# Kernel tuning notes

Measured on AMD Instinct MI355X. Metric: run time of the kernel, lower is better.

Reference implementation:

```python
import jax, jax.numpy as jnp
import numpy as np

B = 16          # number of documents
PREV = 768      # prev_output_size (input embedding dim)
D = 256         # input_size after projection
LENGTHS = np.array([1024 + 128 * i for i in range(B)], dtype=np.int64)  # ragged doc lengths
T = int(LENGTHS.sum())      # 31744 total sentence embeddings
MAXLEN = int(LENGTHS.max()) # 2944 padded sequence length


def setup_inputs() -> dict:
    key = jax.random.key(0)
    k1, k2 = jax.random.split(key, 2)
    sent_embs = jax.random.normal(k1, (T, PREV), dtype=jnp.float32)
    W = jax.random.normal(k2, (PREV, D), dtype=jnp.float32) / np.float32(np.sqrt(PREV))
    b = jnp.zeros((D,), dtype=jnp.float32)
    return {
        "sent_embs": sent_embs,
        "W": W,
        "b": b,
        "lengths": jnp.asarray(LENGTHS),
        "max_len": MAXLEN,
    }


def reference(sent_embs, W, b, lengths, max_len):
    # emb_to_hidden_mapping: Linear(prev_output_size -> input_size)
    x = sent_embs @ W + b                      # [T, D]
    T_ = x.shape[0]
    Bn = lengths.shape[0]
    # Ragged -> padded scatter (replaces the Python index-building loop):
    # exclusive cumsum gives the start offset of each doc inside the concat.
    offs = jnp.concatenate([jnp.zeros((1,), lengths.dtype), jnp.cumsum(lengths)[:-1]])
    batch_ids = jnp.repeat(jnp.arange(Bn), lengths, total_repeat_length=T_)  # [T]
    within = jnp.arange(T_) - offs[batch_ids]                                # position inside doc
    tgt = batch_ids * max_len + within                                       # flat padded row index
    padded = jnp.zeros((Bn * max_len, x.shape[1]), x.dtype).at[tgt].set(x)
    # encoder is an injected opaque module; identity here -> padded seqs
    return padded.reshape(Bn, max_len, x.shape[1])  # [B, max_len, D]
```

## Files before the change

kernel.cpp:

```cpp
#include <hip/hip_runtime.h>
#include <hip/hip_bf16.h>


#define T_TOTAL 31744
#define K_DIM   768
#define N_DIM   256
#define MAXLEN  2944
#define NKT     24
#define NGEMM   496
#define NZERO   240

typedef __attribute__((ext_vector_type(8))) short    bf16x8;
typedef __attribute__((ext_vector_type(4))) float    f32x4;
typedef __attribute__((ext_vector_type(4))) unsigned u32x4;

__device__ __forceinline__ unsigned short f2bf(float f) {
  unsigned u = __builtin_bit_cast(unsigned, f);
  u += 0x7fffu + ((u >> 16) & 1u);
  return (unsigned short)(u >> 16);
}

__device__ __forceinline__ unsigned cvtpk(float lo, float hi) {
  unsigned r;
  asm("v_cvt_pk_bf16_f32 %0, %1, %2" : "=v"(r) : "v"(lo), "v"(hi));
  return r;
}

__device__ __forceinline__ void gload16(const void* g, void* l) {
  __builtin_amdgcn_global_load_lds(
      (const __attribute__((address_space(1))) unsigned int*)g,
      (__attribute__((address_space(3))) unsigned int*)l,
      16, 0, 0);
}

__global__ __launch_bounds__(256) void wt_tile(const float* __restrict__ W,
                                               unsigned short* __restrict__ Wt) {
  __shared__ float Wl[32][257];
  const int kt  = blockIdx.x;
  const int tid = threadIdx.x;

#pragma unroll
  for (int i = 0; i < 8; ++i) {
    const int idx = i * 256 + tid;
    const int row = idx >> 6;
    const int c4  = idx & 63;
    f32x4 v = *(const f32x4*)(W + (size_t)(kt * 32 + row) * N_DIM + c4 * 4);
    Wl[row][c4 * 4 + 0] = v[0];
    Wl[row][c4 * 4 + 1] = v[1];
    Wl[row][c4 * 4 + 2] = v[2];
    Wl[row][c4 * 4 + 3] = v[3];
  }
  __syncthreads();

#pragma unroll
  for (int h = 0; h < 4; ++h) {
    bf16x8 ov;
#pragma unroll
    for (int e = 0; e < 8; ++e) ov[e] = (short)f2bf(Wl[h * 8 + e][tid]);
    *(bf16x8*)(Wt + (((size_t)kt * 4 + h) * 256 + tid) * 8) = ov;
  }
}

__global__ __launch_bounds__(512, 4) void gemm_scatter(const float* __restrict__ A,
                                                       const unsigned short* __restrict__ Wt,
                                                       const float* __restrict__ bias,
                                                       float* __restrict__ out) {
  const int tid = threadIdx.x;

  if (blockIdx.x >= NGEMM) {
    const int z  = blockIdx.x - NGEMM;
    const int p0 = z * 64;
    int d = 0, c = 0;
    while (d < 15) {
      const int pad = 1920 - 128 * d;
      if (p0 < c + pad) break;
      c += pad; ++d;
    }
    const int len = 1024 + 128 * d;
    const size_t row0 = (size_t)d * MAXLEN + len + (p0 - c);
    float* dst = out + row0 * N_DIM;
    const f32x4 z4 = {0.f, 0.f, 0.f, 0.f};
#pragma unroll
    for (int j = 0; j < 8; ++j)
      *(f32x4*)(dst + (size_t)(j * 512 + tid) * 4) = z4;
    return;
  }

  __shared__ f32x4 AbV[2][256];
  __shared__ f32x4 BbV[2][1024];

  const int wid  = tid >> 6;
  const int lane = tid & 63;
  const int l15  = lane & 15;
  const int l4   = lane >> 4;
  const int wr   = wid >> 2;
  const int wc   = wid & 3;
  const int t0   = blockIdx.x * 64;

  int off = 0, doc = 0;
  while (doc < 15) {
    const int len = 1024 + 128 * doc;
    if (t0 < off + len) break;
    off += len; ++doc;
  }
  const long tgt0 = (long)doc * MAXLEN + (t0 - off);

  const int rowS = (tid & 255) >> 2;
  const int gS   = tid & 3;
  const float* pA = A + (size_t)(t0 + rowS) * K_DIM + gS * 8;
  const int awbyte = (gS * 64 + (rowS ^ (gS << 1))) * 16;

  const unsigned short* pB = Wt + (size_t)tid * 8;

  char* ldsA  = (char*)&AbV[0][0];
  char* ldsB  = (char*)&BbV[0][0];
  char* ldsBw = ldsB + wid * 1024;

  const int arow  = wr * 32 + l15;
  const int aoff0 = l4 * 1024 + ((arow ^ (l4 << 1)) * 16);
  const int boff  = l4 * 4096 + (wc * 64 + l15) * 16;

  f32x4 acc[2][4];
#pragma unroll
  for (int m = 0; m < 2; ++m)
#pragma unroll
    for (int n = 0; n < 4; ++n) acc[m][n] = f32x4{0.f, 0.f, 0.f, 0.f};

#define STAGE_B(buf, kt_)                                                \
  {                                                                      \
    gload16(pB + (size_t)(kt_) * 8192, ldsBw + (buf) * 16384);           \
    gload16(pB + (size_t)(kt_) * 8192 + 4096,                            \
            ldsBw + (buf) * 16384 + 8192);                               \
  }

#define WRITE_A(buf, La0, La1)                                           \
  {                                                                      \
    u32x4 u;                                                             \
    u[0] = cvtpk(La0[0], La0[1]); u[1] = cvtpk(La0[2], La0[3]);          \
    u[2] = cvtpk(La1[0], La1[1]); u[3] = cvtpk(La1[2], La1[3]);          \
    *(u32x4*)(ldsA + (buf) * 4096 + awbyte) = u;                         \
  }

#define COMPUTE(buf)                                                     \
  {                                                                      \
    const char* ab = ldsA + (buf) * 4096;                                \
    const char* bb = ldsB + (buf) * 16384 + boff;                        \
    bf16x8 bf0 = *(const bf16x8*)(bb);                                   \
    bf16x8 bf1 = *(const bf16x8*)(bb + 256);                             \
    bf16x8 bf2 = *(const bf16x8*)(bb + 512);                             \
    bf16x8 bf3 = *(const bf16x8*)(bb + 768);                             \
    bf16x8 af0 = *(const bf16x8*)(ab + aoff0);                           \
    bf16x8 af1 = *(const bf16x8*)(ab + aoff0 + 256);                     \
    acc[0][0] = __builtin_amdgcn_mfma_f32_16x16x32_bf16(af0, bf0, acc[0][0], 0, 0, 0); \
    acc[0][1] = __builtin_amdgcn_mfma_f32_16x16x32_bf16(af0, bf1, acc[0][1], 0, 0, 0); \
    acc[0][2] = __builtin_amdgcn_mfma_f32_16x16x32_bf16(af0, bf2, acc[0][2], 0, 0, 0); \
    acc[0][3] = __builtin_amdgcn_mfma_f32_16x16x32_bf16(af0, bf3, acc[0][3], 0, 0, 0); \
    acc[1][0] = __builtin_amdgcn_mfma_f32_16x16x32_bf16(af1, bf0, acc[1][0], 0, 0, 0); \
    acc[1][1] = __builtin_amdgcn_mfma_f32_16x16x32_bf16(af1, bf1, acc[1][1], 0, 0, 0); \
    acc[1][2] = __builtin_amdgcn_mfma_f32_16x16x32_bf16(af1, bf2, acc[1][2], 0, 0, 0); \
    acc[1][3] = __builtin_amdgcn_mfma_f32_16x16x32_bf16(af1, bf3, acc[1][3], 0, 0, 0); \
  }

  if (tid < 256) {
    f32x4 La0 = *(const f32x4*)(pA);
    f32x4 La1 = *(const f32x4*)(pA + 4);
    WRITE_A(0, La0, La1)
  }
  STAGE_B(0, 0)
  __syncthreads();

#pragma unroll 1
  for (int t = 0; t < NKT - 1; ++t) {
    f32x4 La0, La1;
    if (tid < 256) {
      La0 = *(const f32x4*)(pA + (t + 1) * 32);
      La1 = *(const f32x4*)(pA + (t + 1) * 32 + 4);
    }
    STAGE_B((t + 1) & 1, t + 1)
    COMPUTE(t & 1)
    if (tid < 256) WRITE_A((t + 1) & 1, La0, La1)
    __syncthreads();
  }
  COMPUTE((NKT - 1) & 1)

  float bc[4];
#pragma unroll
  for (int n = 0; n < 4; ++n) bc[n] = bias[wc * 64 + n * 16 + l15];

#pragma unroll
  for (int m = 0; m < 2; ++m)
#pragma unroll
    for (int n = 0; n < 4; ++n) {
      const size_t base = (size_t)(tgt0 + wr * 32 + m * 16 + l4 * 4) * N_DIM
                        + wc * 64 + n * 16 + l15;
#pragma unroll
      for (int j = 0; j < 4; ++j)
        out[base + (size_t)j * N_DIM] = acc[m][n][j] + bc[n];
    }
#undef STAGE_B
#undef WRITE_A
#undef COMPUTE
}

extern "C" void kernel_launch(void* const* d_in, const int* in_sizes, int n_in,
                              void* d_out, int out_size, void* d_ws, size_t ws_size,
                              hipStream_t stream) {
  const float* A    = (const float*)d_in[0];
  const float* W    = (const float*)d_in[1];
  const float* bias = (const float*)d_in[2];
  float* out = (float*)d_out;
  unsigned short* Wt = (unsigned short*)d_ws;

  wt_tile<<<24, 256, 0, stream>>>(W, Wt);
  gemm_scatter<<<NGEMM + NZERO, 512, 0, stream>>>(A, Wt, bias, out);
}
```

Baseline: 33.58 us.

## Shrink GEMM tile to 32 rows and load W fragments directly from global

Halves the row tile per block to 32 tokens with 256 threads (4 waves), doubling the GEMM grid. The LDS staging of the bf16 W tile via global_load_lds is removed, and each wave now loads its B fragments straight from global memory (L2-resident) into registers every k-step. This cuts LDS use and barrier work and raises block count for occupancy. The trade-off is more redundant global/L2 traffic for W, since it is no longer shared across waves through LDS, and load latency is exposed in the loop.

```diff
diff --git a/kernel.cpp b/kernel.cpp
--- a/kernel.cpp
+++ b/kernel.cpp
@@ -7,7 +7,7 @@
 #define N_DIM   256
 #define MAXLEN  2944
 #define NKT     24
-#define NGEMM   496
+#define NGEMM   992
 #define NZERO   240
 
 typedef __attribute__((ext_vector_type(8))) short    bf16x8;
@@ -24,13 +24,6 @@
   unsigned r;
   asm("v_cvt_pk_bf16_f32 %0, %1, %2" : "=v"(r) : "v"(lo), "v"(hi));
   return r;
-}
-
-__device__ __forceinline__ void gload16(const void* g, void* l) {
-  __builtin_amdgcn_global_load_lds(
-      (const __attribute__((address_space(1))) unsigned int*)g,
-      (__attribute__((address_space(3))) unsigned int*)l,
-      16, 0, 0);
 }
 
 __global__ __launch_bounds__(256) void wt_tile(const float* __restrict__ W,
@@ -61,7 +54,7 @@
   }
 }
 
-__global__ __launch_bounds__(512, 4) void gemm_scatter(const float* __restrict__ A,
+__global__ __launch_bounds__(256, 4) void gemm_scatter(const float* __restrict__ A,
                                                        const unsigned short* __restrict__ Wt,
                                                        const float* __restrict__ bias,
                                                        float* __restrict__ out) {
@@ -81,21 +74,18 @@
     float* dst = out + row0 * N_DIM;
     const f32x4 z4 = {0.f, 0.f, 0.f, 0.f};
 #pragma unroll
-    for (int j = 0; j < 8; ++j)
-      *(f32x4*)(dst + (size_t)(j * 512 + tid) * 4) = z4;
+    for (int j = 0; j < 16; ++j)
+      *(f32x4*)(dst + (size_t)(j * 256 + tid) * 4) = z4;
     return;
   }
 
-  __shared__ f32x4 AbV[2][256];
-  __shared__ f32x4 BbV[2][1024];
+  __shared__ f32x4 AbV[2][128];
 
   const int wid  = tid >> 6;
   const int lane = tid & 63;
   const int l15  = lane & 15;
   const int l4   = lane >> 4;
-  const int wr   = wid >> 2;
-  const int wc   = wid & 3;
-  const int t0   = blockIdx.x * 64;
+  const int t0   = blockIdx.x * 32;
 
   int off = 0, doc = 0;
   while (doc < 15) {
@@ -105,20 +95,17 @@
   }
   const long tgt0 = (long)doc * MAXLEN + (t0 - off);
 
-  const int rowS = (tid & 255) >> 2;
+  const int rowS = (tid & 127) >> 2;
   const int gS   = tid & 3;
   const float* pA = A + (size_t)(t0 + rowS) * K_DIM + gS * 8;
-  const int awbyte = (gS * 64 + (rowS ^ (gS << 1))) * 16;
+  const int awbyte = (gS * 32 + (rowS ^ (gS << 1))) * 16;
 
-  const unsigned short* pB = Wt + (size_t)tid * 8;
+  const int colB = wid * 64 + l15;
+  const unsigned short* pB = Wt + ((size_t)l4 * 256 + colB) * 8;
 
-  char* ldsA  = (char*)&AbV[0][0];
-  char* ldsB  = (char*)&BbV[0][0];
-  char* ldsBw = ldsB + wid * 1024;
+  char* ldsA = (char*)&AbV[0][0];
 
-  const int arow  = wr * 32 + l15;
-  const int aoff0 = l4 * 1024 + ((arow ^ (l4 << 1)) * 16);
-  const int boff  = l4 * 4096 + (wc * 64 + l15) * 16;
+  const int aoff0 = l4 * 512 + ((l15 ^ (l4 << 1)) * 16);
 
   f32x4 acc[2][4];
 #pragma unroll
@@ -126,80 +113,69 @@
 #pragma unroll
     for (int n = 0; n < 4; ++n) acc[m][n] = f32x4{0.f, 0.f, 0.f, 0.f};
 
-#define STAGE_B(buf, kt_)                                                \
-  {                                                                      \
-    gload16(pB + (size_t)(kt_) * 8192, ldsBw + (buf) * 16384);           \
-    gload16(pB + (size_t)(kt_) * 8192 + 4096,                            \
-            ldsBw + (buf) * 16384 + 8192);                               \
-  }
-
 #define WRITE_A(buf, La0, La1)                                           \
   {                                                                      \
     u32x4 u;                                                             \
     u[0] = cvtpk(La0[0], La0[1]); u[1] = cvtpk(La0[2], La0[3]);          \
     u[2] = cvtpk(La1[0], La1[1]); u[3] = cvtpk(La1[2], La1[3]);          \
-    *(u32x4*)(ldsA + (buf) * 4096 + awbyte) = u;                         \
+    *(u32x4*)(ldsA + (buf) * 2048 + awbyte) = u;                         \
   }
 
-#define COMPUTE(buf)                                                     \
-  {                                                                      \
-    const char* ab = ldsA + (buf) * 4096;                                \
-    const char* bb = ldsB + (buf) * 16384 + boff;                        \
-    bf16x8 bf0 = *(const bf16x8*)(bb);                                   \
-    bf16x8 bf1 = *(const bf16x8*)(bb + 256);                             \
-    bf16x8 bf2 = *(const bf16x8*)(bb + 512);                             \
-    bf16x8 bf3 = *(const bf16x8*)(bb + 768);                             \
-    bf16x8 af0 = *(const bf16x8*)(ab + aoff0);                           \
-    bf16x8 af1 = *(const bf16x8*)(ab + aoff0 + 256);                     \
-    acc[0][0] = __builtin_amdgcn_mfma_f32_16x16x32_bf16(af0, bf0, acc[0][0], 0, 0, 0); \
-    acc[0][1] = __builtin_amdgcn_mfma_f32_16x16x32_bf16(af0, bf1, acc[0][1], 0, 0, 0); \
-    acc[0][2] = __builtin_amdgcn_mfma_f32_16x16x32_bf16(af0, bf2, acc[0][2], 0, 0, 0); \
-    acc[0][3] = __builtin_amdgcn_mfma_f32_16x16x32_bf16(af0, bf3, acc[0][3], 0, 0, 0); \
-    acc[1][0] = __builtin_amdgcn_mfma_f32_16x16x32_bf16(af1, bf0, acc[1][0], 0, 0, 0); \
-    acc[1][1] = __builtin_amdgcn_mfma_f32_16x16x32_bf16(af1, bf1, acc[1][1], 0, 0, 0); \
-    acc[1][2] = __builtin_amdgcn_mfma_f32_16x16x32_bf16(af1, bf2, acc[1][2], 0, 0, 0); \
-    acc[1][3] = __builtin_amdgcn_mfma_f32_16x16x32_bf16(af1, bf3, acc[1][3], 0, 0, 0); \
-  }
-
-  if (tid < 256) {
+  if (tid < 128) {
     f32x4 La0 = *(const f32x4*)(pA);
     f32x4 La1 = *(const f32x4*)(pA + 4);
     WRITE_A(0, La0, La1)
   }
-  STAGE_B(0, 0)
   __syncthreads();
 
 #pragma unroll 1
-  for (int t = 0; t < NKT - 1; ++t) {
+  for (int t = 0; t < NKT; ++t) {
+    const unsigned short* pBt = pB + (size_t)t * 8192;
+    bf16x8 b0 = *(const bf16x8*)(pBt);
+    bf16x8 b1 = *(const bf16x8*)(pBt + 128);
+    bf16x8 b2 = *(const bf16x8*)(pBt + 256);
+    bf16x8 b3 = *(const bf16x8*)(pBt + 384);
+
     f32x4 La0, La1;
-    if (tid < 256) {
+    if (t < NKT - 1 && tid < 128) {
       La0 = *(const f32x4*)(pA + (t + 1) * 32);
       La1 = *(const f32x4*)(pA + (t + 1) * 32 + 4);
     }
-    STAGE_B((t + 1) & 1, t + 1)
-    COMPUTE(t & 1)
-    if (tid < 256) WRITE_A((t + 1) & 1, La0, La1)
-    __syncthreads();
+
+    const char* ab = ldsA + (t & 1) * 2048;
+    bf16x8 af0 = *(const bf16x8*)(ab + aoff0);
+    bf16x8 af1 = *(const bf16x8*)(ab + aoff0 + 256);
+
+    acc[0][0] = __builtin_amdgcn_mfma_f32_16x16x32_bf16(af0, b0, acc[0][0], 0, 0, 0);
+    acc[0][1] = __builtin_amdgcn_mfma_f32_16x16x32_bf16(af0, b1, acc[0][1], 0, 0, 0);
+    acc[0][2] = __builtin_amdgcn_mfma_f32_16x16x32_bf16(af0, b2, acc[0][2], 0, 0, 0);
+    acc[0][3] = __builtin_amdgcn_mfma_f32_16x16x32_bf16(af0, b3, acc[0][3], 0, 0, 0);
+    acc[1][0] = __builtin_amdgcn_mfma_f32_16x16x32_bf16(af1, b0, acc[1][0], 0, 0, 0);
+    acc[1][1] = __builtin_amdgcn_mfma_f32_16x16x32_bf16(af1, b1, acc[1][1], 0, 0, 0);
+    acc[1][2] = __builtin_amdgcn_mfma_f32_16x16x32_bf16(af1, b2, acc[1][2], 0, 0, 0);
+    acc[1][3] = __builtin_amdgcn_mfma_f32_16x16x32_bf16(af1, b3, acc[1][3], 0, 0, 0);
+
+    if (t < NKT - 1) {
+      if (tid < 128) WRITE_A((t + 1) & 1, La0, La1)
+      __syncthreads();
+    }
   }
-  COMPUTE((NKT - 1) & 1)
 
   float bc[4];
 #pragma unroll
-  for (int n = 0; n < 4; ++n) bc[n] = bias[wc * 64 + n * 16 + l15];
+  for (int n = 0; n < 4; ++n) bc[n] = bias[wid * 64 + n * 16 + l15];
 
 #pragma unroll
   for (int m = 0; m < 2; ++m)
 #pragma unroll
     for (int n = 0; n < 4; ++n) {
-      const size_t base = (size_t)(tgt0 + wr * 32 + m * 16 + l4 * 4) * N_DIM
-                        + wc * 64 + n * 16 + l15;
+      const size_t base = (size_t)(tgt0 + m * 16 + l4 * 4) * N_DIM
+                        + wid * 64 + n * 16 + l15;
 #pragma unroll
       for (int j = 0; j < 4; ++j)
         out[base + (size_t)j * N_DIM] = acc[m][n][j] + bc[n];
     }
-#undef STAGE_B
 #undef WRITE_A
-#undef COMPUTE
 }
 
 extern "C" void kernel_launch(void* const* d_in, const int* in_sizes, int n_in,
@@ -212,5 +188,5 @@
   unsigned short* Wt = (unsigned short*)d_ws;
 
   wt_tile<<<24, 256, 0, stream>>>(W, Wt);
-  gemm_scatter<<<NGEMM + NZERO, 512, 0, stream>>>(A, Wt, bias, out);
+  gemm_scatter<<<NGEMM + NZERO, 256, 0, stream>>>(A, Wt, bias, out);
 }
```

Measured after the change: 36.50 us. 8.7% more time.

## Double GEMM row tile to 128 rows per block with 4x4 MFMA per wave

Applied to the files above, without the earlier changes.

Each GEMM block now covers 128 token rows instead of 64, so the GEMM grid is halved. All 512 threads load the fp32 activations, and each wave runs a 4x4 grid of MFMA tiles per k-step. The LDS A buffer and its swizzle are widened to match, and the occupancy hint drops from 4 to 2 blocks. The aim is to reuse each staged bf16 W tile across twice as many rows, cutting L2 traffic for W and barrier overhead per row. The costs are fewer blocks (248 GEMM blocks on a 256-CU part), higher register use and lower occupancy, which can hurt latency hiding in what is largely a memory-bound kernel.

```diff
diff --git a/kernel.cpp b/kernel.cpp
--- a/kernel.cpp
+++ b/kernel.cpp
@@ -7,7 +7,7 @@
 #define N_DIM   256
 #define MAXLEN  2944
 #define NKT     24
-#define NGEMM   496
+#define NGEMM   248
 #define NZERO   240
 
 typedef __attribute__((ext_vector_type(8))) short    bf16x8;
@@ -61,7 +61,7 @@
   }
 }
 
-__global__ __launch_bounds__(512, 4) void gemm_scatter(const float* __restrict__ A,
+__global__ __launch_bounds__(512, 2) void gemm_scatter(const float* __restrict__ A,
                                                        const unsigned short* __restrict__ Wt,
                                                        const float* __restrict__ bias,
                                                        float* __restrict__ out) {
@@ -86,7 +86,7 @@
     return;
   }
 
-  __shared__ f32x4 AbV[2][256];
+  __shared__ f32x4 AbV[2][512];
   __shared__ f32x4 BbV[2][1024];
 
   const int wid  = tid >> 6;
@@ -95,7 +95,7 @@
   const int l4   = lane >> 4;
   const int wr   = wid >> 2;
   const int wc   = wid & 3;
-  const int t0   = blockIdx.x * 64;
+  const int t0   = blockIdx.x * 128;
 
   int off = 0, doc = 0;
   while (doc < 15) {
@@ -105,10 +105,10 @@
   }
   const long tgt0 = (long)doc * MAXLEN + (t0 - off);
 
-  const int rowS = (tid & 255) >> 2;
+  const int rowS = tid >> 2;
   const int gS   = tid & 3;
   const float* pA = A + (size_t)(t0 + rowS) * K_DIM + gS * 8;
-  const int awbyte = (gS * 64 + (rowS ^ (gS << 1))) * 16;
+  const int awbyte = (gS * 128 + (rowS ^ (gS << 1))) * 16;
 
   const unsigned short* pB = Wt + (size_t)tid * 8;
 
@@ -116,16 +116,28 @@
   char* ldsB  = (char*)&BbV[0][0];
   char* ldsBw = ldsB + wid * 1024;
 
-  const int arow  = wr * 32 + l15;
-  const int aoff0 = l4 * 1024 + ((arow ^ (l4 << 1)) * 16);
+  const int arowb = wr * 64 + l15;
+  const int abase = (l4 * 128 + (arowb ^ (l4 << 1))) * 16;
   const int boff  = l4 * 4096 + (wc * 64 + l15) * 16;
 
-  f32x4 acc[2][4];
-#pragma unroll
-  for (int m = 0; m < 2; ++m)
+  f32x4 acc[4][4];
+#pragma unroll
+  for (int m = 0; m < 4; ++m)
 #pragma unroll
     for (int n = 0; n < 4; ++n) acc[m][n] = f32x4{0.f, 0.f, 0.f, 0.f};
 
+#define LOAD_A(t_, La0, La1)                                             \
+  {                                                                      \
+    La0 = *(const f32x4*)(pA + (t_) * 32);                               \
+    La1 = *(const f32x4*)(pA + (t_) * 32 + 4);                           \
+  }
+#define WRITE_A(buf, La0, La1)                                           \
+  {                                                                      \
+    u32x4 u;                                                             \
+    u[0] = cvtpk(La0[0], La0[1]); u[1] = cvtpk(La0[2], La0[3]);          \
+    u[2] = cvtpk(La1[0], La1[1]); u[3] = cvtpk(La1[2], La1[3]);          \
+    *(u32x4*)(ldsA + (buf) * 8192 + awbyte) = u;                         \
+  }
 #define STAGE_B(buf, kt_)                                                \
   {                                                                      \
     gload16(pB + (size_t)(kt_) * 8192, ldsBw + (buf) * 16384);           \
@@ -133,52 +145,36 @@
             ldsBw + (buf) * 16384 + 8192);                               \
   }
 
-#define WRITE_A(buf, La0, La1)                                           \
-  {                                                                      \
-    u32x4 u;                                                             \
-    u[0] = cvtpk(La0[0], La0[1]); u[1] = cvtpk(La0[2], La0[3]);          \
-    u[2] = cvtpk(La1[0], La1[1]); u[3] = cvtpk(La1[2], La1[3]);          \
-    *(u32x4*)(ldsA + (buf) * 4096 + awbyte) = u;                         \
-  }
-
 #define COMPUTE(buf)                                                     \
   {                                                                      \
-    const char* ab = ldsA + (buf) * 4096;                                \
+    const char* ab = ldsA + (buf) * 8192 + abase;                        \
     const char* bb = ldsB + (buf) * 16384 + boff;                        \
-    bf16x8 bf0 = *(const bf16x8*)(bb);                                   \
-    bf16x8 bf1 = *(const bf16x8*)(bb + 256);                             \
-    bf16x8 bf2 = *(const bf16x8*)(bb + 512);                             \
-    bf16x8 bf3 = *(const bf16x8*)(bb + 768);                             \
-    bf16x8 af0 = *(const bf16x8*)(ab + aoff0);                           \
-    bf16x8 af1 = *(const bf16x8*)(ab + aoff0 + 256);                     \
-    acc[0][0] = __builtin_amdgcn_mfma_f32_16x16x32_bf16(af0, bf0, acc[0][0], 0, 0, 0); \
-    acc[0][1] = __builtin_amdgcn_mfma_f32_16x16x32_bf16(af0, bf1, acc[0][1], 0, 0, 0); \
-    acc[0][2] = __builtin_amdgcn_mfma_f32_16x16x32_bf16(af0, bf2, acc[0][2], 0, 0, 0); \
-    acc[0][3] = __builtin_amdgcn_mfma_f32_16x16x32_bf16(af0, bf3, acc[0][3], 0, 0, 0); \
-    acc[1][0] = __builtin_amdgcn_mfma_f32_16x16x32_bf16(af1, bf0, acc[1][0], 0, 0, 0); \
-    acc[1][1] = __builtin_amdgcn_mfma_f32_16x16x32_bf16(af1, bf1, acc[1][1], 0, 0, 0); \
-    acc[1][2] = __builtin_amdgcn_mfma_f32_16x16x32_bf16(af1, bf2, acc[1][2], 0, 0, 0); \
-    acc[1][3] = __builtin_amdgcn_mfma_f32_16x16x32_bf16(af1, bf3, acc[1][3], 0, 0, 0); \
-  }
-
-  if (tid < 256) {
-    f32x4 La0 = *(const f32x4*)(pA);
-    f32x4 La1 = *(const f32x4*)(pA + 4);
+    bf16x8 bfr[4], afr[4];                                               \
+    _Pragma("unroll") for (int n = 0; n < 4; ++n)                        \
+      bfr[n] = *(const bf16x8*)(bb + n * 256);                           \
+    _Pragma("unroll") for (int m = 0; m < 4; ++m)                        \
+      afr[m] = *(const bf16x8*)(ab + m * 256);                           \
+    _Pragma("unroll") for (int m = 0; m < 4; ++m)                        \
+      _Pragma("unroll") for (int n = 0; n < 4; ++n)                      \
+        acc[m][n] = __builtin_amdgcn_mfma_f32_16x16x32_bf16(afr[m], bfr[n], \
+                                                            acc[m][n], 0, 0, 0); \
+  }
+
+  {
+    f32x4 La0, La1;
+    LOAD_A(0, La0, La1)
+    STAGE_B(0, 0)
     WRITE_A(0, La0, La1)
   }
-  STAGE_B(0, 0)
   __syncthreads();
 
 #pragma unroll 1
   for (int t = 0; t < NKT - 1; ++t) {
     f32x4 La0, La1;
-    if (tid < 256) {
-      La0 = *(const f32x4*)(pA + (t + 1) * 32);
-      La1 = *(const f32x4*)(pA + (t + 1) * 32 + 4);
-    }
+    LOAD_A(t + 1, La0, La1)
     STAGE_B((t + 1) & 1, t + 1)
     COMPUTE(t & 1)
-    if (tid < 256) WRITE_A((t + 1) & 1, La0, La1)
+    WRITE_A((t + 1) & 1, La0, La1)
     __syncthreads();
   }
   COMPUTE((NKT - 1) & 1)
@@ -188,17 +184,18 @@
   for (int n = 0; n < 4; ++n) bc[n] = bias[wc * 64 + n * 16 + l15];
 
 #pragma unroll
-  for (int m = 0; m < 2; ++m)
+  for (int m = 0; m < 4; ++m)
 #pragma unroll
     for (int n = 0; n < 4; ++n) {
-      const size_t base = (size_t)(tgt0 + wr * 32 + m * 16 + l4 * 4) * N_DIM
+      const size_t base = (size_t)(tgt0 + wr * 64 + m * 16 + l4 * 4) * N_DIM
                         + wc * 64 + n * 16 + l15;
 #pragma unroll
       for (int j = 0; j < 4; ++j)
         out[base + (size_t)j * N_DIM] = acc[m][n][j] + bc[n];
     }
+#undef LOAD_A
+#undef WRITE_A
 #undef STAGE_B
-#undef WRITE_A
 #undef COMPUTE
 }
 
```

New measurement: 45.31 us. 34.9% more time.

## Triple-buffer W tiles in LDS with manual waitcnt and barriers

Applied to the files above, without the earlier changes.

The B (weight) operand moves from double to triple buffering in LDS. Each W k-tile is now prefetched two iterations ahead, and __syncthreads is replaced by explicit lgkmcnt waits, s_barrier and sched_barrier fences, so the global-to-LDS loads get more time to land behind the MFMA work. In exchange, per-block LDS grows from about 40KB to 56KB, which can cut how many blocks fit per CU. The loop also no longer waits explicitly on vmcnt for the in-flight LDS-direct loads, which risks a race on threads that do not load A.

```diff
diff --git a/kernel.cpp b/kernel.cpp
--- a/kernel.cpp
+++ b/kernel.cpp
@@ -87,7 +87,7 @@
   }
 
   __shared__ f32x4 AbV[2][256];
-  __shared__ f32x4 BbV[2][1024];
+  __shared__ f32x4 BbV[3][1024];
 
   const int wid  = tid >> 6;
   const int lane = tid & 63;
@@ -141,10 +141,10 @@
     *(u32x4*)(ldsA + (buf) * 4096 + awbyte) = u;                         \
   }
 
-#define COMPUTE(buf)                                                     \
+#define COMPUTE(abuf, bbuf)                                              \
   {                                                                      \
-    const char* ab = ldsA + (buf) * 4096;                                \
-    const char* bb = ldsB + (buf) * 16384 + boff;                        \
+    const char* ab = ldsA + (abuf) * 4096;                               \
+    const char* bb = ldsB + (bbuf) * 16384 + boff;                       \
     bf16x8 bf0 = *(const bf16x8*)(bb);                                   \
     bf16x8 bf1 = *(const bf16x8*)(bb + 256);                             \
     bf16x8 bf2 = *(const bf16x8*)(bb + 512);                             \
@@ -161,13 +161,23 @@
     acc[1][3] = __builtin_amdgcn_mfma_f32_16x16x32_bf16(af1, bf3, acc[1][3], 0, 0, 0); \
   }
 
-  if (tid < 256) {
-    f32x4 La0 = *(const f32x4*)(pA);
-    f32x4 La1 = *(const f32x4*)(pA + 4);
-    WRITE_A(0, La0, La1)
-  }
-  STAGE_B(0, 0)
-  __syncthreads();
+  {
+    f32x4 La0, La1;
+    if (tid < 256) {
+      La0 = *(const f32x4*)(pA);
+      La1 = *(const f32x4*)(pA + 4);
+    }
+    __builtin_amdgcn_sched_barrier(0);
+    STAGE_B(0, 0)
+    STAGE_B(1, 1)
+    __builtin_amdgcn_sched_barrier(0);
+    if (tid < 256) WRITE_A(0, La0, La1)
+    asm volatile("s_waitcnt vmcnt(2)" ::: "memory");
+    asm volatile("s_waitcnt lgkmcnt(0)" ::: "memory");
+    __builtin_amdgcn_sched_barrier(0);
+    __builtin_amdgcn_s_barrier();
+    __builtin_amdgcn_sched_barrier(0);
+  }
 
 #pragma unroll 1
   for (int t = 0; t < NKT - 1; ++t) {
@@ -176,12 +186,17 @@
       La0 = *(const f32x4*)(pA + (t + 1) * 32);
       La1 = *(const f32x4*)(pA + (t + 1) * 32 + 4);
     }
-    STAGE_B((t + 1) & 1, t + 1)
-    COMPUTE(t & 1)
+    __builtin_amdgcn_sched_barrier(0);
+    if (t + 2 < NKT) STAGE_B((t + 2) % 3, t + 2)
+    __builtin_amdgcn_sched_barrier(0);
+    COMPUTE(t & 1, t % 3)
     if (tid < 256) WRITE_A((t + 1) & 1, La0, La1)
-    __syncthreads();
-  }
-  COMPUTE((NKT - 1) & 1)
+    asm volatile("s_waitcnt lgkmcnt(0)" ::: "memory");
+    __builtin_amdgcn_sched_barrier(0);
+    __builtin_amdgcn_s_barrier();
+    __builtin_amdgcn_sched_barrier(0);
+  }
+  COMPUTE((NKT - 1) & 1, (NKT - 1) % 3)
 
   float bc[4];
 #pragma unroll
```

New measurement: 34.80 us. +3.6%, slower.
